# Kernel optimization log

Hardware: AMD Instinct MI355X
Metric: run time of the kernel (lower is better)

## Reference

```python
import jax, jax.numpy as jnp
import numpy as np

N = 50000          # nodes
E = 800000         # directed edges (before self-loops)
HID = 64           # hidden_dim
HEADS = 4          # conv1 heads
NUM_CLASSES = 16
SLOPE = 0.2        # PyG GATConv default negative_slope


def setup_inputs() -> dict:
    key = jax.random.key(0)
    ks = jax.random.split(key, 10)
    s1 = 1.0 / np.sqrt(HID)
    s2 = 1.0 / np.sqrt(HEADS * HID)
    return {
        "x": jax.random.normal(ks[0], (N, HID), jnp.float32),
        "edge_index": jax.random.randint(ks[1], (2, E), 0, N, dtype=jnp.int64),
        # conv1: GATConv(64 -> 64, heads=4, concat)
        "W1": jax.random.normal(ks[2], (HID, HEADS * HID), jnp.float32) * s1,
        "att_src1": jax.random.normal(ks[3], (HEADS, HID), jnp.float32) * s1,
        "att_dst1": jax.random.normal(ks[4], (HEADS, HID), jnp.float32) * s1,
        "b1": jnp.zeros((HEADS * HID,), jnp.float32),
        # conv2: GATConv(256 -> num_classes, heads=1, concat)
        "W2": jax.random.normal(ks[5], (HEADS * HID, NUM_CLASSES), jnp.float32) * s2,
        "att_src2": jax.random.normal(ks[6], (1, NUM_CLASSES), jnp.float32) * s2,
        "att_dst2": jax.random.normal(ks[7], (1, NUM_CLASSES), jnp.float32) * s2,
        "b2": jnp.zeros((NUM_CLASSES,), jnp.float32),
    }


def _gat_conv(x, src, dst, W, att_s, att_d, b, heads, out_dim):
    # x: [N, F_in]; src/dst: [E'] with self-loops (PyG add_self_loops=True)
    xh = (x @ W).reshape(-1, heads, out_dim)                 # [N, H, D]
    a_src = jnp.einsum('nhd,hd->nh', xh, att_s)              # [N, H]
    a_dst = jnp.einsum('nhd,hd->nh', xh, att_d)              # [N, H]
    e = a_src[src] + a_dst[dst]                              # [E', H]
    e = jnp.where(e > 0, e, SLOPE * e)                       # leaky_relu(0.2)
    # segment softmax over incoming edges of each dst node
    m = jax.lax.stop_gradient(jax.ops.segment_max(e, dst, num_segments=N))
    ex = jnp.exp(e - m[dst])
    denom = jax.ops.segment_sum(ex, dst, num_segments=N)
    alpha = ex / (denom[dst] + 1e-16)                        # [E', H]
    out = jax.ops.segment_sum(xh[src] * alpha[:, :, None], dst, num_segments=N)
    return out.reshape(N, heads * out_dim) + b


def reference(x, edge_index, W1, att_src1, att_dst1, b1, W2, att_src2, att_dst2, b2):
    loops = jnp.arange(N, dtype=edge_index.dtype)
    src = jnp.concatenate([edge_index[0], loops])
    dst = jnp.concatenate([edge_index[1], loops])
    h = _gat_conv(x, src, dst, W1, att_src1, att_dst1, b1, HEADS, HID)
    h = jax.nn.elu(h)
    # F.dropout(p=0.5, training=False) -> identity at inference
    h = _gat_conv(h, src, dst, W2, att_src2, att_dst2, b2, 1, NUM_CLASSES)
    return jax.nn.log_softmax(h, axis=1)
```

## Files before the change

kernel.cpp:

```cpp
#include <hip/hip_runtime.h>
#include <hip/hip_bf16.h>
#include <math.h>

#define N_NODES 50000
#define N_EDGES 800000
#define EP (N_EDGES + N_NODES)
#define HID 64
#define HEADS 4
#define F1 (HEADS * HID)
#define NC 16
#define SLOPE 0.2f
#define G1B 1024
#define NT 49

__device__ __forceinline__ unsigned short bf16rn(float f) {
    unsigned u = __float_as_uint(f);
    return (unsigned short)((u + 0x7fffu + ((u >> 16) & 1u)) >> 16);
}
__device__ __forceinline__ float bf_lo(unsigned p) { return __uint_as_float(p << 16); }
__device__ __forceinline__ float bf_hi(unsigned p) { return __uint_as_float(p & 0xffff0000u); }

__device__ __forceinline__ void edge_sd(int e, const int* __restrict__ ei, int& s, int& d) {
    if (e < N_EDGES) { s = ei[e]; d = ei[N_EDGES + e]; }
    else             { s = e - N_EDGES; d = s; }
}

__global__ __launch_bounds__(1024) void k_scan_local(const int* __restrict__ cnt,
        int* __restrict__ lexcl, int* __restrict__ bsum) {
    __shared__ int wsum[16];
    int t = threadIdx.x, lane = t & 63, wid = t >> 6;
    int i = blockIdx.x * 1024 + t;
    int v = (i < N_NODES) ? cnt[i] : 0;
    int s = v;
#pragma unroll
    for (int off = 1; off < 64; off <<= 1) {
        int x = __shfl_up(s, off);
        if (lane >= off) s += x;
    }
    if (lane == 63) wsum[wid] = s;
    __syncthreads();
    if (t < 16) {
        int w = wsum[t];
#pragma unroll
        for (int off = 1; off < 16; off <<= 1) {
            int x = __shfl_up(w, off);
            if (t >= off) w += x;
        }
        wsum[t] = w;
    }
    __syncthreads();
    int waveoff = (wid == 0) ? 0 : wsum[wid - 1];
    int incl = s + waveoff;
    if (i < N_NODES) lexcl[i] = incl - v;
    if (t == 1023) bsum[blockIdx.x] = incl;
}

__global__ __launch_bounds__(256) void k_scan_add(int* __restrict__ row_start,
        const int* __restrict__ bsum, int* __restrict__ cursor) {
    __shared__ int sb[64];
    __shared__ int stot;
    int t = threadIdx.x;
    if (t < 64) {
        int v = (t < NT) ? bsum[t] : 0;
        int s = v;
#pragma unroll
        for (int off = 1; off < 64; off <<= 1) {
            int x = __shfl_up(s, off);
            if (t >= off) s += x;
        }
        sb[t] = s - v;
        if (t == 63) stot = s;
    }
    __syncthreads();
    int i = blockIdx.x * 256 + t;
    if (i < N_NODES) {
        int v = row_start[i] + sb[i >> 10];
        row_start[i] = v;
        cursor[i] = v;
    }
    if (i == 0) row_start[N_NODES] = stot;
}

__global__ void k_scatter(const int* __restrict__ ei, int* __restrict__ cursor,
                          int* __restrict__ esrc) {
    int e = blockIdx.x * blockDim.x + threadIdx.x;
    if (e >= EP) return;
    int s, d; edge_sd(e, ei, s, d);
    int p = atomicAdd(&cursor[d], 1);
    esrc[p] = s;
}

__global__ __launch_bounds__(256) void k_gemm1(
        const float* __restrict__ x, const float* __restrict__ W1,
        const float* __restrict__ att_s, const float* __restrict__ att_d,
        unsigned short* __restrict__ xh1b, float* __restrict__ a_src, float* __restrict__ a_dst,
        const int* __restrict__ ei, int* __restrict__ cnt) {
    for (int e = blockIdx.x * 256 + threadIdx.x; e < EP; e += 256 * G1B) {
        int s, d; edge_sd(e, ei, s, d);
        atomicAdd(&cnt[d], 1);
    }
    int t = threadIdx.x;
    float w[HID];
#pragma unroll
    for (int k = 0; k < HID; ++k) w[k] = W1[k * F1 + t];
    float as_ = att_s[t], ad_ = att_d[t];
    __shared__ float xs[8][HID];
    int b = blockIdx.x;
    for (int i0 = 0; i0 < 49; i0 += 8) {
        __syncthreads();
        int col = t & 63;
#pragma unroll
        for (int half = 0; half < 2; ++half) {
            int rr = (t >> 6) + half * 4;
            int r = b + (i0 + rr) * G1B;
            if (r < N_NODES) xs[rr][col] = x[(size_t)r * HID + col];
        }
        __syncthreads();
#pragma unroll
        for (int rr = 0; rr < 8; ++rr) {
            int r = b + (i0 + rr) * G1B;
            if (r >= N_NODES) continue;
            const float4* xr = (const float4*)xs[rr];
            float acc = 0.0f;
#pragma unroll
            for (int q = 0; q < 16; ++q) {
                float4 xv = xr[q];
                acc += w[4*q] * xv.x + w[4*q+1] * xv.y + w[4*q+2] * xv.z + w[4*q+3] * xv.w;
            }
            xh1b[(size_t)r * F1 + t] = bf16rn(acc);
            float ps = acc * as_, pd = acc * ad_;
#pragma unroll
            for (int o = 32; o >= 1; o >>= 1) {
                ps += __shfl_xor(ps, o);
                pd += __shfl_xor(pd, o);
            }
            if ((t & 63) == 0) {
                int h = t >> 6;
                a_src[r * HEADS + h] = ps;
                a_dst[r * HEADS + h] = pd;
            }
        }
    }
}

__global__ __launch_bounds__(256) void k_csr1(
        const int* __restrict__ row_start, const int* __restrict__ esrc,
        const float* __restrict__ a_src, const float* __restrict__ a_dst,
        const unsigned short* __restrict__ xh1b, const float* __restrict__ b1,
        const float* __restrict__ W2, const float* __restrict__ att_s2,
        const float* __restrict__ att_d2,
        unsigned short* __restrict__ xh2b, float* __restrict__ a_src2,
        float* __restrict__ a_dst2) {
    int w = threadIdx.x >> 6, l = threadIdx.x & 63;
    int d = blockIdx.x * 4 + w;
    if (d >= N_NODES) return;
    int base = row_start[d], deg = row_start[d + 1] - base;
    __shared__ int   ls[4][64];
    __shared__ float lal[4][4][64];
    int h = l >> 4, e16 = l & 15;
    int* lsw = ls[w];
    float adh = a_dst[d * HEADS + h];
    float m = -1e30f, den = 0.0f;
    float a0 = 0.0f, a1 = 0.0f, a2 = 0.0f, a3 = 0.0f;
    for (int c0 = 0; c0 < deg; c0 += 64) {
        int cn = min(64, deg - c0);
        if (l < cn) lsw[l] = esrc[base + c0 + l];
        float cm = -1e30f;
        for (int j = e16; j < cn; j += 16) {
            float ev = a_src[lsw[j] * HEADS + h] + adh;
            ev = ev > 0.0f ? ev : SLOPE * ev;
            lal[w][h][j] = ev;
            cm = fmaxf(cm, ev);
        }
#pragma unroll
        for (int o = 8; o >= 1; o >>= 1) cm = fmaxf(cm, __shfl_xor(cm, o));
        float mn = fmaxf(m, cm);
        float sc = expf(m - mn);
        a0 *= sc; a1 *= sc; a2 *= sc; a3 *= sc; den *= sc; m = mn;
        float cs = 0.0f;
        for (int j = e16; j < cn; j += 16) {
            float wj = expf(lal[w][h][j] - m);
            lal[w][h][j] = wj;
            cs += wj;
        }
#pragma unroll
        for (int o = 8; o >= 1; o >>= 1) cs += __shfl_xor(cs, o);
        den += cs;
        const float* lalh = lal[w][h];
        int j = 0;
        for (; j + 1 < cn; j += 2) {
            float w0 = lalh[j], w1 = lalh[j + 1];
            uint2 p0 = *(const uint2*)(xh1b + (size_t)lsw[j]     * F1 + 4 * l);
            uint2 p1 = *(const uint2*)(xh1b + (size_t)lsw[j + 1] * F1 + 4 * l);
            a0 += w0 * bf_lo(p0.x); a1 += w0 * bf_hi(p0.x);
            a2 += w0 * bf_lo(p0.y); a3 += w0 * bf_hi(p0.y);
            a0 += w1 * bf_lo(p1.x); a1 += w1 * bf_hi(p1.x);
            a2 += w1 * bf_lo(p1.y); a3 += w1 * bf_hi(p1.y);
        }
        if (j < cn) {
            float w0 = lalh[j];
            uint2 p0 = *(const uint2*)(xh1b + (size_t)lsw[j] * F1 + 4 * l);
            a0 += w0 * bf_lo(p0.x); a1 += w0 * bf_hi(p0.x);
            a2 += w0 * bf_lo(p0.y); a3 += w0 * bf_hi(p0.y);
        }
    }
    float inv = 1.0f / (den + 1e-16f);
    float4 bb = *(const float4*)(b1 + 4 * l);
    float v0 = a0 * inv + bb.x;
    float v1 = a1 * inv + bb.y;
    float v2 = a2 * inv + bb.z;
    float v3 = a3 * inv + bb.w;
    v0 = v0 > 0.0f ? v0 : (expf(v0) - 1.0f);
    v1 = v1 > 0.0f ? v1 : (expf(v1) - 1.0f);
    v2 = v2 > 0.0f ? v2 : (expf(v2) - 1.0f);
    v3 = v3 > 0.0f ? v3 : (expf(v3) - 1.0f);
    float* hrow = &lal[w][0][0];
    *(float4*)(hrow + 4 * l) = make_float4(v0, v1, v2, v3);
    int k0 = l >> 2;
    int cg = (l & 3) * 4;
    const float4* w4 = (const float4*)W2;
    float q0 = 0.0f, q1 = 0.0f, q2 = 0.0f, q3 = 0.0f;
#pragma unroll
    for (int j = 0; j < 16; ++j) {
        float hk = hrow[k0 + 16 * j];
        float4 wv = w4[l + 64 * j];
        q0 += hk * wv.x; q1 += hk * wv.y; q2 += hk * wv.z; q3 += hk * wv.w;
    }
#pragma unroll
    for (int o = 4; o <= 32; o <<= 1) {
        q0 += __shfl_xor(q0, o); q1 += __shfl_xor(q1, o);
        q2 += __shfl_xor(q2, o); q3 += __shfl_xor(q3, o);
    }
    if (l < 4) {
        unsigned u0 = (unsigned)bf16rn(q0) | ((unsigned)bf16rn(q1) << 16);
        unsigned u1 = (unsigned)bf16rn(q2) | ((unsigned)bf16rn(q3) << 16);
        *(uint2*)(xh2b + (size_t)d * NC + 4 * l) = make_uint2(u0, u1);
        float ps = q0 * att_s2[cg] + q1 * att_s2[cg + 1]
                 + q2 * att_s2[cg + 2] + q3 * att_s2[cg + 3];
        float pd = q0 * att_d2[cg] + q1 * att_d2[cg + 1]
                 + q2 * att_d2[cg + 2] + q3 * att_d2[cg + 3];
        ps += __shfl_xor(ps, 1); ps += __shfl_xor(ps, 2);
        pd += __shfl_xor(pd, 1); pd += __shfl_xor(pd, 2);
        if (l == 0) { a_src2[d] = ps; a_dst2[d] = pd; }
    }
}

__global__ __launch_bounds__(256) void k_csr2(
        const int* __restrict__ row_start, const int* __restrict__ esrc,
        const float* __restrict__ a_src2, const float* __restrict__ a_dst2,
        const unsigned short* __restrict__ xh2b, const float* __restrict__ b2,
        float* __restrict__ out) {
    int w = threadIdx.x >> 6, l = threadIdx.x & 63;
    int d = blockIdx.x * 4 + w;
    if (d >= N_NODES) return;
    int base = row_start[d], deg = row_start[d + 1] - base;
    __shared__ int   ls[4][64];
    __shared__ float lal[4][64];
    float adh = a_dst2[d];
    int cp = l & 7, je = l >> 3;
    float denl = 0.0f, acc0 = 0.0f, acc1 = 0.0f;
    for (int c0 = 0; c0 < deg; c0 += 64) {
        int cn = min(64, deg - c0);
        if (l < cn) {
            int s = esrc[base + c0 + l];
            ls[w][l] = s;
            float ev = a_src2[s] + adh;
            ev = ev > 0.0f ? ev : SLOPE * ev;
            float wj = __expf(ev);
            lal[w][l] = wj;
            denl += wj;
        }
        for (int j = je; j < cn; j += 8) {
            float wj = lal[w][j];
            unsigned pv = *(const unsigned*)(xh2b + (size_t)ls[w][j] * NC + 2 * cp);
            acc0 += wj * bf_lo(pv);
            acc1 += wj * bf_hi(pv);
        }
    }
#pragma unroll
    for (int o = 32; o >= 1; o >>= 1) denl += __shfl_xor(denl, o);
#pragma unroll
    for (int o = 8; o <= 32; o <<= 1) {
        acc0 += __shfl_xor(acc0, o);
        acc1 += __shfl_xor(acc1, o);
    }
    float inv = 1.0f / (denl + 1e-16f);
    float v0 = acc0 * inv + b2[2 * cp];
    float v1 = acc1 * inv + b2[2 * cp + 1];
    float mm = fmaxf(v0, v1);
#pragma unroll
    for (int o = 1; o <= 4; o <<= 1) mm = fmaxf(mm, __shfl_xor(mm, o));
    float se = __expf(v0 - mm) + __expf(v1 - mm);
#pragma unroll
    for (int o = 1; o <= 4; o <<= 1) se += __shfl_xor(se, o);
    float lse = mm + logf(se);
    if (l < 8) *(float2*)(out + (size_t)d * NC + 2 * cp) = make_float2(v0 - lse, v1 - lse);
}

extern "C" void kernel_launch(void* const* d_in, const int* in_sizes, int n_in,
                              void* d_out, int out_size, void* d_ws, size_t ws_size,
                              hipStream_t stream) {
    const float* x        = (const float*)d_in[0];
    const int*   ei       = (const int*)d_in[1];
    const float* W1       = (const float*)d_in[2];
    const float* att_src1 = (const float*)d_in[3];
    const float* att_dst1 = (const float*)d_in[4];
    const float* b1       = (const float*)d_in[5];
    const float* W2       = (const float*)d_in[6];
    const float* att_src2 = (const float*)d_in[7];
    const float* att_dst2 = (const float*)d_in[8];
    const float* b2       = (const float*)d_in[9];
    float* out = (float*)d_out;

    char* p = (char*)d_ws;
    unsigned short* xh1b  = (unsigned short*)p; p += (size_t)N_NODES * F1 * 2;
    unsigned short* xh2b  = (unsigned short*)p; p += (size_t)N_NODES * NC * 2;
    float* a_src1 = (float*)p; p += (size_t)N_NODES * HEADS * 4;
    float* a_dst1 = (float*)p; p += (size_t)N_NODES * HEADS * 4;
    float* a_src2 = (float*)p; p += (size_t)N_NODES * 4;
    float* a_dst2 = (float*)p; p += (size_t)N_NODES * 4;
    int* cnt       = (int*)p;  p += (size_t)N_NODES * 4;
    int* cursor    = (int*)p;  p += (size_t)N_NODES * 4;
    int* row_start = (int*)p;  p += (size_t)(N_NODES + 1) * 4;
    int* bsum      = (int*)p;  p += 64 * 4;
    int* esrc      = (int*)p;  p += (size_t)EP * 4;

    hipMemsetAsync(cnt, 0, (size_t)N_NODES * 4, stream);
    k_gemm1<<<G1B, 256, 0, stream>>>(x, W1, att_src1, att_dst1, xh1b, a_src1, a_dst1,
                                     ei, cnt);
    k_scan_local<<<NT, 1024, 0, stream>>>(cnt, row_start, bsum);
    k_scan_add<<<(N_NODES + 255) / 256, 256, 0, stream>>>(row_start, bsum, cursor);
    k_scatter<<<(EP + 255) / 256, 256, 0, stream>>>(ei, cursor, esrc);

    k_csr1<<<(N_NODES + 3) / 4, 256, 0, stream>>>(row_start, esrc, a_src1, a_dst1, xh1b, b1,
                                                  W2, att_src2, att_dst2, xh2b, a_src2, a_dst2);

    k_csr2<<<(N_NODES + 3) / 4, 256, 0, stream>>>(row_start, esrc, a_src2, a_dst2, xh2b, b2, out);
}
```

Baseline: 253.6 us.

## Use bf16 MFMA for first-layer projection with 16-row tiles

Replaces the scalar FP32 dot-product GEMM in k_gemm1 with bf16 MFMA 16x16x32 instructions. W1 fragments are held in registers and each block processes 16-row tiles of x staged through padded shared memory. The grid is halved to 512 blocks. Inputs x and W1 are now rounded to bf16 before multiplication, which lowers precision of xh1 and the attention logits compared with FP32 accumulation on FP32 inputs.

```diff
diff --git a/kernel.cpp b/kernel.cpp
--- a/kernel.cpp
+++ b/kernel.cpp
@@ -10,8 +10,12 @@
 #define F1 (HEADS * HID)
 #define NC 16
 #define SLOPE 0.2f
-#define G1B 1024
+#define NRT 3125
+#define GMB 512
 #define NT 49
+
+typedef __attribute__((ext_vector_type(8))) short short8;
+typedef __attribute__((ext_vector_type(4))) float f32x4;
 
 __device__ __forceinline__ unsigned short bf16rn(float f) {
     unsigned u = __float_as_uint(f);
@@ -95,49 +99,74 @@
         const float* __restrict__ att_s, const float* __restrict__ att_d,
         unsigned short* __restrict__ xh1b, float* __restrict__ a_src, float* __restrict__ a_dst,
         const int* __restrict__ ei, int* __restrict__ cnt) {
-    for (int e = blockIdx.x * 256 + threadIdx.x; e < EP; e += 256 * G1B) {
+    __shared__ float xs[16][68];
+    int t = threadIdx.x;
+    for (int e = blockIdx.x * 256 + t; e < EP; e += 256 * GMB) {
         int s, d; edge_sd(e, ei, s, d);
         atomicAdd(&cnt[d], 1);
     }
-    int t = threadIdx.x;
-    float w[HID];
-#pragma unroll
-    for (int k = 0; k < HID; ++k) w[k] = W1[k * F1 + t];
-    float as_ = att_s[t], ad_ = att_d[t];
-    __shared__ float xs[8][HID];
-    int b = blockIdx.x;
-    for (int i0 = 0; i0 < 49; i0 += 8) {
+    int w = t >> 6, l = t & 63;
+    int lo16 = l & 15, kg = l >> 4;
+    short8 bfrag[4][2];
+#pragma unroll
+    for (int ct = 0; ct < 4; ++ct)
+#pragma unroll
+        for (int kh = 0; kh < 2; ++kh) {
+            const float* wp = W1 + (size_t)(kh * 32 + kg * 8) * F1 + (w * 64 + ct * 16 + lo16);
+            short8 f;
+#pragma unroll
+            for (int i = 0; i < 8; ++i) f[i] = (short)bf16rn(wp[(size_t)i * F1]);
+            bfrag[ct][kh] = f;
+        }
+    float asv[4], adv[4];
+#pragma unroll
+    for (int ct = 0; ct < 4; ++ct) {
+        asv[ct] = att_s[w * 64 + ct * 16 + lo16];
+        adv[ct] = att_d[w * 64 + ct * 16 + lo16];
+    }
+    int sr = t >> 4, sc = (t & 15) * 4;
+    for (int rt = blockIdx.x; rt < NRT; rt += GMB) {
         __syncthreads();
-        int col = t & 63;
-#pragma unroll
-        for (int half = 0; half < 2; ++half) {
-            int rr = (t >> 6) + half * 4;
-            int r = b + (i0 + rr) * G1B;
-            if (r < N_NODES) xs[rr][col] = x[(size_t)r * HID + col];
-        }
+        *(float4*)&xs[sr][sc] = *(const float4*)(x + (size_t)(rt * 16 + sr) * HID + sc);
         __syncthreads();
-#pragma unroll
-        for (int rr = 0; rr < 8; ++rr) {
-            int r = b + (i0 + rr) * G1B;
-            if (r >= N_NODES) continue;
-            const float4* xr = (const float4*)xs[rr];
-            float acc = 0.0f;
-#pragma unroll
-            for (int q = 0; q < 16; ++q) {
-                float4 xv = xr[q];
-                acc += w[4*q] * xv.x + w[4*q+1] * xv.y + w[4*q+2] * xv.z + w[4*q+3] * xv.w;
-            }
-            xh1b[(size_t)r * F1 + t] = bf16rn(acc);
-            float ps = acc * as_, pd = acc * ad_;
-#pragma unroll
-            for (int o = 32; o >= 1; o >>= 1) {
+        short8 af[2];
+#pragma unroll
+        for (int kh = 0; kh < 2; ++kh) {
+            const float* xp = &xs[lo16][kh * 32 + kg * 8];
+            float4 u0 = *(const float4*)xp;
+            float4 u1 = *(const float4*)(xp + 4);
+            short8 f;
+            f[0] = (short)bf16rn(u0.x); f[1] = (short)bf16rn(u0.y);
+            f[2] = (short)bf16rn(u0.z); f[3] = (short)bf16rn(u0.w);
+            f[4] = (short)bf16rn(u1.x); f[5] = (short)bf16rn(u1.y);
+            f[6] = (short)bf16rn(u1.z); f[7] = (short)bf16rn(u1.w);
+            af[kh] = f;
+        }
+        f32x4 acc[4];
+#pragma unroll
+        for (int ct = 0; ct < 4; ++ct) {
+            acc[ct] = (f32x4){0.f, 0.f, 0.f, 0.f};
+            acc[ct] = __builtin_amdgcn_mfma_f32_16x16x32_bf16(af[0], bfrag[ct][0], acc[ct], 0, 0, 0);
+            acc[ct] = __builtin_amdgcn_mfma_f32_16x16x32_bf16(af[1], bfrag[ct][1], acc[ct], 0, 0, 0);
+        }
+#pragma unroll
+        for (int reg = 0; reg < 4; ++reg) {
+            int gr = rt * 16 + kg * 4 + reg;
+#pragma unroll
+            for (int ct = 0; ct < 4; ++ct)
+                xh1b[(size_t)gr * F1 + w * 64 + ct * 16 + lo16] = bf16rn(acc[ct][reg]);
+            float ps = acc[0][reg] * asv[0] + acc[1][reg] * asv[1]
+                     + acc[2][reg] * asv[2] + acc[3][reg] * asv[3];
+            float pd = acc[0][reg] * adv[0] + acc[1][reg] * adv[1]
+                     + acc[2][reg] * adv[2] + acc[3][reg] * adv[3];
+#pragma unroll
+            for (int o = 1; o <= 8; o <<= 1) {
                 ps += __shfl_xor(ps, o);
                 pd += __shfl_xor(pd, o);
             }
-            if ((t & 63) == 0) {
-                int h = t >> 6;
-                a_src[r * HEADS + h] = ps;
-                a_dst[r * HEADS + h] = pd;
+            if (lo16 == 0) {
+                a_src[gr * HEADS + w] = ps;
+                a_dst[gr * HEADS + w] = pd;
             }
         }
     }
@@ -326,7 +355,7 @@
     int* esrc      = (int*)p;  p += (size_t)EP * 4;
 
     hipMemsetAsync(cnt, 0, (size_t)N_NODES * 4, stream);
-    k_gemm1<<<G1B, 256, 0, stream>>>(x, W1, att_src1, att_dst1, xh1b, a_src1, a_dst1,
+    k_gemm1<<<GMB, 256, 0, stream>>>(x, W1, att_src1, att_dst1, xh1b, a_src1, a_dst1,
                                      ei, cnt);
     k_scan_local<<<NT, 1024, 0, stream>>>(cnt, row_start, bsum);
     k_scan_add<<<(N_NODES + 255) / 256, 256, 0, stream>>>(row_start, bsum, cursor);
```

Measured after the change: 214.7 us. 15.3% less time.
